# Kernel tuning notes

Hardware: AMD Instinct MI355X
Metric: run time of the kernel (lower is better)

The kernel has to match this reference:

```python
import jax, jax.numpy as jnp
import numpy as np

SHUFFLE_G = 8
NUM_HEADS = 8
EPS = 1e-12


def setup_inputs() -> dict:
    key = jax.random.key(0)
    ks = jax.random.split(key, 7)
    b, dim, t, h, w = 2, 64, 10, 128, 128
    c3 = dim * 3
    return {
        "x": jax.random.normal(ks[0], (b, dim, t, h, w), jnp.float32),
        "W1": jax.random.normal(ks[1], (c3, dim), jnp.float32) * 0.05,            # 1x1x1 conv
        "Wdw": jax.random.normal(ks[2], (c3, 1, 1, 3, 3), jnp.float32) * 0.1,     # depthwise (1,3,3) conv
        "W_lin": jax.random.normal(ks[3], (t * SHUFFLE_G, t * SHUFFLE_G), jnp.float32) * 0.05,
        "b_lin": jax.random.normal(ks[4], (t * SHUFFLE_G,), jnp.float32) * 0.01,
        "temperature": jnp.ones((NUM_HEADS, 1, 1), jnp.float32),
        "W_out": jax.random.normal(ks[5], (dim, dim), jnp.float32) * 0.05,        # 1x1x1 conv
    }


def _l2norm(v):
    n = jnp.sqrt(jnp.sum(v * v, axis=-1, keepdims=True))
    return v / jnp.maximum(n, EPS)


def reference(x, W1, Wdw, W_lin, b_lin, temperature, W_out):
    b, c, t, h, w = x.shape
    c3 = 3 * c
    heads = NUM_HEADS
    # 1x1x1 pointwise conv (no bias)
    y = jnp.einsum('oc,bcthw->bothw', W1, x)
    # depthwise (1,3,3) conv, padding (0,1,1)
    y = jax.lax.conv_general_dilated(
        y, Wdw, window_strides=(1, 1, 1),
        padding=((0, 0), (1, 1), (1, 1)),
        dimension_numbers=('NCDHW', 'OIDHW', 'NCDHW'),
        feature_group_count=c3)
    # shuffle: b (c1 c2) t h w -> b c2 h w (c1 t), c1 = SHUFFLE_G
    c1, c2 = SHUFFLE_G, c3 // SHUFFLE_G
    y = y.reshape(b, c1, c2, t, h, w).transpose(0, 2, 4, 5, 1, 3).reshape(b, c2, h, w, c1 * t)
    # linear mixing along (c1 t)
    y = jnp.einsum('bchwi,oi->bchwo', y, W_lin) + b_lin
    # unshuffle: b c2 h w (c1 t) -> b (c2 c1 t) h w
    y = y.reshape(b, c2, h, w, c1, t).transpose(0, 1, 4, 5, 2, 3).reshape(b, c3 * t, h, w)
    # split qkv along channel
    q, k, v = jnp.split(y, 3, axis=1)  # each [b, c*t, h, w]
    ct, hw = (c // heads) * t, h * w
    q = q.reshape(b, heads, ct, hw)
    k = k.reshape(b, heads, ct, hw)
    v = v.reshape(b, heads, ct, hw)
    q = _l2norm(q)
    k = _l2norm(k)
    attn = jnp.einsum('bhcd,bhed->bhce', q, k) * temperature  # [b, heads, ct, ct]
    attn = jax.nn.softmax(attn, axis=-1)
    out = jnp.einsum('bhce,bhed->bhcd', attn, v)  # [b, heads, ct, hw]
    out = out.reshape(b, c, t, h, w)
    out = jnp.einsum('oc,bcthw->bothw', W_out, out)
    return out
```

## Files before the change

### kernel.cpp

```cpp
#include <hip/hip_runtime.h>
#include <hip/hip_bf16.h>

#define C_  64
#define C3_ 192
#define T_  10
#define H_  128
#define W_  128
#define HW_ 16384
#define THW_ 163840
#define NH_ 8
#define C2_ 24
#define TG_ 80

typedef __hip_bfloat16 bf16;
typedef __attribute__((ext_vector_type(8))) short bf16x8;
typedef __attribute__((ext_vector_type(4))) float f32x4;

__device__ __forceinline__ float bf2f(bf16 v) { return __bfloat162float(v); }

__device__ __forceinline__ ushort f2bf_s(float f) {
  bf16 h = __float2bfloat16(f);
  union { bf16 b; ushort s; } u; u.b = h; return u.s;
}

__device__ __forceinline__ ushort4 pack4(f32x4 a) {
  ushort4 p;
  p.x = f2bf_s(a[0]); p.y = f2bf_s(a[1]); p.z = f2bf_s(a[2]); p.w = f2bf_s(a[3]);
  return p;
}

__device__ __forceinline__ uint pack2lo(uint x, uint y) { return (x & 0xffffu) | (y << 16); }
__device__ __forceinline__ uint pack2hi(uint x, uint y) { return (x >> 16) | (y & 0xffff0000u); }

__device__ __forceinline__ void twrite(char* lds, int stride, int nkc,
                                       uint r[8][4], int kc, int cg) {
#pragma unroll
  for (int j = 0; j < 8; ++j) {
    const int d = j >> 1;
    uint4 o;
    if (j & 1) {
      o.x = pack2hi(r[0][d], r[1][d]); o.y = pack2hi(r[2][d], r[3][d]);
      o.z = pack2hi(r[4][d], r[5][d]); o.w = pack2hi(r[6][d], r[7][d]);
    } else {
      o.x = pack2lo(r[0][d], r[1][d]); o.y = pack2lo(r[2][d], r[3][d]);
      o.z = pack2lo(r[4][d], r[5][d]); o.w = pack2lo(r[6][d], r[7][d]);
    }
    const int col = cg * 8 + j;
    const int rr = (kc + col) % nkc;
    *reinterpret_cast<uint4*>(lds + col * stride + rr * 16) = o;
  }
}

__global__ __launch_bounds__(256) void kprep(
    const float* __restrict__ W1, const float* __restrict__ W_lin,
    const float* __restrict__ W_out,
    bf16* __restrict__ W1bf, bf16* __restrict__ Wlinbf, bf16* __restrict__ Woutbf) {
  const int idx = blockIdx.x * 256 + threadIdx.x;
  if (idx < 12288) {
    W1bf[idx] = __float2bfloat16(W1[idx]);
  } else if (idx < 12288 + 7680) {
    const int i = idx - 12288;
    const int row = i / 96, col = i - row * 96;
    Wlinbf[i] = __float2bfloat16(col < 80 ? W_lin[row * 80 + col] : 0.f);
  } else if (idx < 12288 + 7680 + 4096) {
    const int i = idx - 12288 - 7680;
    Woutbf[i] = __float2bfloat16(W_out[i]);
  }
}

#define K1_TPB 4
__global__ __launch_bounds__(256) void k1_mfma(
    const float* __restrict__ x, const bf16* __restrict__ W1bf,
    bf16* __restrict__ y1ws) {
  __shared__ __align__(16) float xs[2][64 * 128];
  const int tid = threadIdx.x;
  const int lane = tid & 63, wv = tid >> 6;
  const int lr = lane & 15, lg = lane >> 4;
  const int mh = blockIdx.y;
  const int b = blockIdx.z;
  const float* xb = x + (size_t)b * C_ * THW_;
  bf16* y1 = y1ws + (size_t)b * C3_ * THW_;
  const int tile0 = blockIdx.x * K1_TPB;

  const int ro = lane >> 5, colo = (lane & 31) * 4;
  auto STAGE = [&](int buf, int tIdx) {
    const int n0 = tIdx * 128;
#pragma unroll
    for (int i = 0; i < 8; ++i) {
      const int row = wv * 16 + i * 2;
      const float* gsrc = xb + (size_t)(row + ro) * THW_ + n0 + colo;
      __builtin_amdgcn_global_load_lds(
          (const __attribute__((address_space(1))) void*)gsrc,
          (__attribute__((address_space(3))) void*)&xs[buf][row * 128],
          16, 0, 0);
    }
  };

  STAGE(0, tile0);

  bf16x8 wf[6][2];
#pragma unroll
  for (int mt = 0; mt < 6; ++mt)
#pragma unroll
    for (int c = 0; c < 2; ++c) {
      const int row = mh * 96 + mt * 16 + lr;
      wf[mt][c] = *reinterpret_cast<const bf16x8*>(W1bf + row * 64 + c * 32 + lg * 8);
    }
  __syncthreads();

  int buf = 0;
  for (int t = 0; t < K1_TPB; ++t) {
    if (t + 1 < K1_TPB) STAGE(buf ^ 1, tile0 + t + 1);
    const int n0 = (tile0 + t) * 128;
#pragma unroll
    for (int nt = 0; nt < 2; ++nt) {
      const int col = wv * 32 + nt * 16 + lr;
      bf16x8 xa[2];
#pragma unroll
      for (int c = 0; c < 2; ++c) {
        const float* base = &xs[buf][(c * 32 + lg * 8) * 128 + col];
        bf16x8 f;
#pragma unroll
        for (int e = 0; e < 8; ++e) f[e] = f2bf_s(base[e * 128]);
        xa[c] = f;
      }
      f32x4 acc[6];
#pragma unroll
      for (int mt = 0; mt < 6; ++mt) acc[mt] = (f32x4){0.f, 0.f, 0.f, 0.f};
#pragma unroll
      for (int c = 0; c < 2; ++c)
#pragma unroll
        for (int mt = 0; mt < 6; ++mt)
          acc[mt] = __builtin_amdgcn_mfma_f32_16x16x32_bf16(xa[c], wf[mt][c], acc[mt], 0, 0, 0);
      const int nb = n0 + wv * 32 + nt * 16 + lg * 4;
#pragma unroll
      for (int mt = 0; mt < 6; ++mt) {
        const int o = mh * 96 + mt * 16 + lr;
        *reinterpret_cast<ushort4*>(y1 + (size_t)o * THW_ + nb) = pack4(acc[mt]);
      }
    }
    __syncthreads();
    buf ^= 1;
  }
}

__global__ __launch_bounds__(256) void k2_dw(
    const bf16* __restrict__ y1ws, const float* __restrict__ Wdw,
    bf16* __restrict__ y2ws) {
  __shared__ float tile[34][132];
  const int tid = threadIdx.x;
  const int blk = blockIdx.x;
  const int b = blockIdx.y;
  const bf16* y1 = y1ws + (size_t)b * C3_ * THW_;
  bf16* y2 = y2ws + (size_t)b * C3_ * THW_;
  const int hs = (blk & 3) * 32;
  const int rest = blk >> 2;
  const int t = rest % T_;
  const int o = rest / T_;
  const bf16* src = y1 + ((size_t)o * T_ + t) * HW_;

  if (tid < 68) {
    const int r = tid >> 1, side = tid & 1;
    tile[r][side ? 129 : 0] = 0.f;
  }
  {
    const int rr = tid >> 5, c4 = (tid & 31) * 4;
#pragma unroll
    for (int p = 0; p < 5; ++p) {
      const int r = p * 8 + rr;
      if (r < 34) {
        const int hh = hs - 1 + r;
        float e0 = 0.f, e1 = 0.f, e2 = 0.f, e3 = 0.f;
        if (hh >= 0 && hh < H_) {
          uint2 raw = *reinterpret_cast<const uint2*>(src + hh * W_ + c4);
          e0 = __uint_as_float(raw.x << 16);
          e1 = __uint_as_float(raw.x & 0xffff0000u);
          e2 = __uint_as_float(raw.y << 16);
          e3 = __uint_as_float(raw.y & 0xffff0000u);
        }
        tile[r][1 + c4]     = e0;
        tile[r][1 + c4 + 1] = e1;
        tile[r][1 + c4 + 2] = e2;
        tile[r][1 + c4 + 3] = e3;
      }
    }
  }
  __syncthreads();

  float kk[9];
#pragma unroll
  for (int i = 0; i < 9; ++i) kk[i] = Wdw[o * 9 + i];

  bf16* dst = y2 + ((size_t)o * T_ + t) * HW_;
  const int w = tid & 127;
  const int r0 = (tid >> 7) * 16;

  float a[3][3];
#pragma unroll
  for (int ky = 0; ky < 3; ++ky)
#pragma unroll
    for (int kx = 0; kx < 3; ++kx) a[ky][kx] = tile[r0 + ky][w + kx];

#pragma unroll
  for (int q = 0; q < 16; ++q) {
    float acc = 0.f;
#pragma unroll
    for (int ky = 0; ky < 3; ++ky)
#pragma unroll
      for (int kx = 0; kx < 3; ++kx)
        acc = fmaf(kk[ky * 3 + kx], a[ky][kx], acc);
    dst[(hs + r0 + q) * W_ + w] = __float2bfloat16(acc);
    if (q < 15) {
#pragma unroll
      for (int kx = 0; kx < 3; ++kx) {
        a[0][kx] = a[1][kx];
        a[1][kx] = a[2][kx];
        a[2][kx] = tile[r0 + q + 3][w + kx];
      }
    }
  }
}

#define K3_NKC 13
#define K3_STRIDE 208
#define K3_TPB 4
__global__ __launch_bounds__(256) void k3_mfma(
    const bf16* __restrict__ y2ws, const bf16* __restrict__ Wlinbf,
    const float* __restrict__ b_lin, bf16* __restrict__ zws,
    float* __restrict__ ssqws) {
  __shared__ __align__(16) char lds[256 * K3_STRIDE];
  const int tid = threadIdx.x;
  const int tile0 = blockIdx.x * K3_TPB;
  const int c2 = blockIdx.y;
  const int b = blockIdx.z;
  const bf16* y2 = y2ws + (size_t)b * C3_ * THW_;
  bf16* z = zws + (size_t)b * C3_ * THW_;
  float* ssq = ssqws + b * 1280;

  const int lane = tid & 63, wv = tid >> 6;
  const int lr = lane & 15, lg = lane >> 4;

  const int kcA = tid >> 5, cgA = tid & 31;
  const bool hasB = (tid & 3) == 0;
  const int qB = tid >> 2;
  const int kcB = 8 + (qB >> 5), cgB = qB & 31;

  uint rrA[8][4], rrB[8][4];
  auto LOAD = [&](int s0, uint r[8][4], int kc, int cg) {
#pragma unroll
    for (int e = 0; e < 8; ++e) {
      const int k = kc * 8 + e;
      const int c1 = (k * 205) >> 11;
      const int tt = k - c1 * 10;
      uint4 raw = *reinterpret_cast<const uint4*>(
          y2 + ((size_t)((c1 * C2_ + c2) * T_ + tt)) * HW_ + s0 + cg * 8);
      r[e][0] = raw.x; r[e][1] = raw.y; r[e][2] = raw.z; r[e][3] = raw.w;
    }
  };

  LOAD(tile0 * 256, rrA, kcA, cgA);
  if (hasB) LOAD(tile0 * 256, rrB, kcB, cgB);
  {
    const int col = tid;
    const uint4 zero4 = {0, 0, 0, 0};
    *reinterpret_cast<uint4*>(lds + col * K3_STRIDE + ((10 + col) % K3_NKC) * 16) = zero4;
    *reinterpret_cast<uint4*>(lds + col * K3_STRIDE + ((11 + col) % K3_NKC) * 16) = zero4;
  }

  bf16x8 wf[5][3];
#pragma unroll
  for (int mt = 0; mt < 5; ++mt)
#pragma unroll
    for (int c = 0; c < 3; ++c)
      wf[mt][c] = *reinterpret_cast<const bf16x8*>(
          Wlinbf + (mt * 16 + lr) * 96 + c * 32 + lg * 8);
  float bias[5];
#pragma unroll
  for (int mt = 0; mt < 5; ++mt) bias[mt] = b_lin[mt * 16 + lr];

  float sqp[5] = {0.f, 0.f, 0.f, 0.f, 0.f};

#pragma unroll
  for (int t = 0; t < K3_TPB; ++t) {
    const int s0 = (tile0 + t) * 256;
    twrite(lds, K3_STRIDE, K3_NKC, rrA, kcA, cgA);
    if (hasB) twrite(lds, K3_STRIDE, K3_NKC, rrB, kcB, cgB);
    if (t + 1 < K3_TPB) {
      LOAD(s0 + 256, rrA, kcA, cgA);
      if (hasB) LOAD(s0 + 256, rrB, kcB, cgB);
    }
    __syncthreads();

    for (int nt = 0; nt < 4; ++nt) {
      const int col = wv * 64 + nt * 16 + lr;
      bf16x8 xa[3];
#pragma unroll
      for (int c = 0; c < 3; ++c) {
        const int kc = c * 4 + lg;
        xa[c] = *reinterpret_cast<const bf16x8*>(
            lds + col * K3_STRIDE + ((kc + col) % K3_NKC) * 16);
      }
      f32x4 acc[5];
#pragma unroll
      for (int mt = 0; mt < 5; ++mt)
        acc[mt] = (f32x4){bias[mt], bias[mt], bias[mt], bias[mt]};
#pragma unroll
      for (int c = 0; c < 3; ++c)
#pragma unroll
        for (int mt = 0; mt < 5; ++mt)
          acc[mt] = __builtin_amdgcn_mfma_f32_16x16x32_bf16(xa[c], wf[mt][c], acc[mt], 0, 0, 0);
      const int sb = s0 + wv * 64 + nt * 16 + lg * 4;
#pragma unroll
      for (int mt = 0; mt < 5; ++mt) {
        const int u = c2 * TG_ + mt * 16 + lr;
        *reinterpret_cast<ushort4*>(z + (size_t)u * HW_ + sb) = pack4(acc[mt]);
#pragma unroll
        for (int j = 0; j < 4; ++j)
          sqp[mt] = fmaf(acc[mt][j], acc[mt][j], sqp[mt]);
      }
    }
    __syncthreads();
  }

  if (c2 < 16) {
#pragma unroll
    for (int mt = 0; mt < 5; ++mt) {
      float v = sqp[mt];
      v += __shfl_xor(v, 16);
      v += __shfl_xor(v, 32);
      if (lane < 16)
        atomicAdd(&ssq[c2 * TG_ + mt * 16 + lane], v);
    }
  }
}

__global__ __launch_bounds__(256) void k5_mfma(
    const bf16* __restrict__ zws, float* __restrict__ Gpartws) {
  __shared__ __align__(16) float gbuf[2][TG_ * TG_];
  const int chunk = blockIdx.x, h = blockIdx.y, b = blockIdx.z;
  const bf16* z = zws + (size_t)b * C3_ * THW_;
  float* Gpart = Gpartws + (size_t)b * 1638400;
  const int tid = threadIdx.x;
  const int lane = tid & 63, wv = tid >> 6;
  const int lr = lane & 15, lg = lane >> 4;

  const bf16* qbase = z + (size_t)(h * TG_) * HW_;
  const bf16* kbase = z + (size_t)((8 + h) * TG_) * HW_;

  f32x4 acc[5][5];
#pragma unroll
  for (int a = 0; a < 5; ++a)
#pragma unroll
    for (int b2 = 0; b2 < 5; ++b2) acc[a][b2] = (f32x4){0.f, 0.f, 0.f, 0.f};

  const int s0 = chunk * 512 + wv * 128;
  for (int s = s0; s < s0 + 128; s += 32) {
    bf16x8 qa[5], kb[5];
#pragma unroll
    for (int a = 0; a < 5; ++a)
      qa[a] = *reinterpret_cast<const bf16x8*>(qbase + (size_t)(a * 16 + lr) * HW_ + s + lg * 8);
#pragma unroll
    for (int a = 0; a < 5; ++a)
      kb[a] = *reinterpret_cast<const bf16x8*>(kbase + (size_t)(a * 16 + lr) * HW_ + s + lg * 8);
#pragma unroll
    for (int a = 0; a < 5; ++a)
#pragma unroll
      for (int b2 = 0; b2 < 5; ++b2)
        acc[a][b2] = __builtin_amdgcn_mfma_f32_16x16x32_bf16(qa[a], kb[b2], acc[a][b2], 0, 0, 0);
  }

  if (wv == 1 || wv == 3) {
    float* dst = gbuf[wv >> 1];
#pragma unroll
    for (int a = 0; a < 5; ++a)
#pragma unroll
      for (int b2 = 0; b2 < 5; ++b2)
#pragma unroll
        for (int j = 0; j < 4; ++j)
          dst[(a * 16 + lg * 4 + j) * TG_ + b2 * 16 + lr] = acc[a][b2][j];
  }
  __syncthreads();
  if (wv == 0 || wv == 2) {
    const float* srcb = gbuf[wv >> 1];
#pragma unroll
    for (int a = 0; a < 5; ++a)
#pragma unroll
      for (int b2 = 0; b2 < 5; ++b2)
#pragma unroll
        for (int j = 0; j < 4; ++j)
          acc[a][b2][j] += srcb[(a * 16 + lg * 4 + j) * TG_ + b2 * 16 + lr];
  }
  __syncthreads();
  if (wv == 2) {
#pragma unroll
    for (int a = 0; a < 5; ++a)
#pragma unroll
      for (int b2 = 0; b2 < 5; ++b2)
#pragma unroll
        for (int j = 0; j < 4; ++j)
          gbuf[0][(a * 16 + lg * 4 + j) * TG_ + b2 * 16 + lr] = acc[a][b2][j];
  }
  __syncthreads();
  if (wv == 0) {
    float* gp = Gpart + ((size_t)chunk * 8 + h) * TG_ * TG_;
#pragma unroll
    for (int a = 0; a < 5; ++a)
#pragma unroll
      for (int b2 = 0; b2 < 5; ++b2)
#pragma unroll
        for (int j = 0; j < 4; ++j) {
          const int i = a * 16 + lg * 4 + j, jj = b2 * 16 + lr;
          gp[i * TG_ + jj] = acc[a][b2][j] + gbuf[0][i * TG_ + jj];
        }
  }
}

__global__ __launch_bounds__(128) void k6_softmax(
    const float* __restrict__ Gpartws, const float* __restrict__ ssqws,
    const float* __restrict__ temp, bf16* __restrict__ attnbfws) {
  __shared__ float red[128];
  __shared__ float smax, ssum;
  const int b = blockIdx.y;
  const float* Gpart = Gpartws + (size_t)b * 1638400;
  const float* ssq = ssqws + b * 1280;
  bf16* attnbf = attnbfws + (size_t)b * NH_ * TG_ * 96;
  int h = blockIdx.x / TG_, i = blockIdx.x % TG_;
  int j = threadIdx.x;
  float logit = -1e30f;
  if (j < TG_) {
    float g = 0.f;
    for (int c = 0; c < 32; ++c)
      g += Gpart[(((size_t)c * 8 + h) * TG_ + i) * TG_ + j];
    float nq = ssq[h * TG_ + i];
    float nk = ssq[(8 + h) * TG_ + j];
    float sq = 1.f / fmaxf(sqrtf(nq), 1e-12f);
    float sk = 1.f / fmaxf(sqrtf(nk), 1e-12f);
    logit = g * sq * sk * temp[h];
  }
  red[j] = logit;
  __syncthreads();
  if (j == 0) {
    float m = -1e30f;
    for (int x2 = 0; x2 < TG_; ++x2) m = fmaxf(m, red[x2]);
    smax = m;
  }
  __syncthreads();
  float e = (j < TG_) ? expf(logit - smax) : 0.f;
  red[j] = e;
  __syncthreads();
  if (j == 0) {
    float s = 0.f;
    for (int x2 = 0; x2 < TG_; ++x2) s += red[x2];
    ssum = s;
  }
  __syncthreads();
  if (j < 96)
    attnbf[((size_t)h * TG_ + i) * 96 + j] =
        __float2bfloat16(j < TG_ ? e / ssum : 0.f);
}

#define K7A_TPB 4
__global__ __launch_bounds__(256) void k7a_mfma(
    const bf16* __restrict__ zws, const bf16* __restrict__ attnbfws,
    bf16* __restrict__ att_outws) {
  __shared__ __align__(16) char lds[256 * K3_STRIDE];
  const int tid = threadIdx.x;
  const int tile0 = blockIdx.x * K7A_TPB;
  const int h = blockIdx.y;
  const int b = blockIdx.z;
  const bf16* z = zws + (size_t)b * C3_ * THW_;
  const bf16* attnbf = attnbfws + (size_t)b * NH_ * TG_ * 96;
  bf16* att_out = att_outws + (size_t)b * NH_ * TG_ * HW_;
  const int voff = (16 + h) * TG_;

  const int lane = tid & 63, wv = tid >> 6;
  const int lr = lane & 15, lg = lane >> 4;

  const int kcA = tid >> 5, cgA = tid & 31;
  const bool hasB = (tid & 3) == 0;
  const int qB = tid >> 2;
  const int kcB = 8 + (qB >> 5), cgB = qB & 31;

  uint rrA[8][4], rrB[8][4];
  auto LOAD = [&](int s0, uint r[8][4], int kc, int cg) {
#pragma unroll
    for (int e = 0; e < 8; ++e) {
      uint4 raw = *reinterpret_cast<const uint4*>(
          z + (size_t)(voff + kc * 8 + e) * HW_ + s0 + cg * 8);
      r[e][0] = raw.x; r[e][1] = raw.y; r[e][2] = raw.z; r[e][3] = raw.w;
    }
  };

  LOAD(tile0 * 256, rrA, kcA, cgA);
  if (hasB) LOAD(tile0 * 256, rrB, kcB, cgB);
  {
    const int col = tid;
    const uint4 zero4 = {0, 0, 0, 0};
    *reinterpret_cast<uint4*>(lds + col * K3_STRIDE + ((10 + col) % K3_NKC) * 16) = zero4;
    *reinterpret_cast<uint4*>(lds + col * K3_STRIDE + ((11 + col) % K3_NKC) * 16) = zero4;
  }

  bf16x8 wf[5][3];
#pragma unroll
  for (int mt = 0; mt < 5; ++mt)
#pragma unroll
    for (int c = 0; c < 3; ++c)
      wf[mt][c] = *reinterpret_cast<const bf16x8*>(
          attnbf + ((size_t)h * TG_ + mt * 16 + lr) * 96 + c * 32 + lg * 8);

#pragma unroll
  for (int t = 0; t < K7A_TPB; ++t) {
    const int s0 = (tile0 + t) * 256;
    twrite(lds, K3_STRIDE, K3_NKC, rrA, kcA, cgA);
    if (hasB) twrite(lds, K3_STRIDE, K3_NKC, rrB, kcB, cgB);
    if (t + 1 < K7A_TPB) {
      LOAD(s0 + 256, rrA, kcA, cgA);
      if (hasB) LOAD(s0 + 256, rrB, kcB, cgB);
    }
    __syncthreads();

    for (int nt = 0; nt < 4; ++nt) {
      const int col = wv * 64 + nt * 16 + lr;
      bf16x8 xa[3];
#pragma unroll
      for (int c = 0; c < 3; ++c) {
        const int kc = c * 4 + lg;
        xa[c] = *reinterpret_cast<const bf16x8*>(
            lds + col * K3_STRIDE + ((kc + col) % K3_NKC) * 16);
      }
      f32x4 acc[5];
#pragma unroll
      for (int mt = 0; mt < 5; ++mt) acc[mt] = (f32x4){0.f, 0.f, 0.f, 0.f};
#pragma unroll
      for (int c = 0; c < 3; ++c)
#pragma unroll
        for (int mt = 0; mt < 5; ++mt)
          acc[mt] = __builtin_amdgcn_mfma_f32_16x16x32_bf16(xa[c], wf[mt][c], acc[mt], 0, 0, 0);
      const int sb = s0 + wv * 64 + nt * 16 + lg * 4;
#pragma unroll
      for (int mt = 0; mt < 5; ++mt) {
        const int u = h * TG_ + mt * 16 + lr;
        *reinterpret_cast<ushort4*>(att_out + (size_t)u * HW_ + sb) = pack4(acc[mt]);
      }
    }
    __syncthreads();
  }
}

#define K1_NKC 10
#define K1_STRIDE 160
#define K7B_TPB 4
__global__ __launch_bounds__(256) void k7b_mfma(
    const bf16* __restrict__ att_outws, const bf16* __restrict__ Woutbf,
    float* __restrict__ out) {
  __shared__ __align__(16) char lds[256 * K1_STRIDE];
  const int tid = threadIdx.x;
  const int tile0 = blockIdx.x * K7B_TPB;
  const int b = blockIdx.y;
  const bf16* att_out = att_outws + (size_t)b * NH_ * TG_ * HW_;
  float* outb = out + (size_t)b * C_ * THW_;
  const int t_ = tile0 >> 6;
  const int lane = tid & 63, wv = tid >> 6;
  const int lr = lane & 15, lg = lane >> 4;

  const int kcA = tid >> 5, cgA = tid & 31;
  uint rrA[8][4];
  auto LOAD = [&](int tile, uint r[8][4]) {
    const int sb0 = (tile * 256) & (HW_ - 1);
#pragma unroll
    for (int e = 0; e < 8; ++e) {
      const int row = kcA * TG_ + e * T_ + t_;
      uint4 raw = *reinterpret_cast<const uint4*>(
          att_out + (size_t)row * HW_ + sb0 + cgA * 8);
      r[e][0] = raw.x; r[e][1] = raw.y; r[e][2] = raw.z; r[e][3] = raw.w;
    }
  };

  LOAD(tile0, rrA);

  bf16x8 wf[4][2];
#pragma unroll
  for (int mt = 0; mt < 4; ++mt)
#pragma unroll
    for (int c = 0; c < 2; ++c)
      wf[mt][c] = *reinterpret_cast<const bf16x8*>(
          Woutbf + (mt * 16 + lr) * 64 + c * 32 + lg * 8);

#pragma unroll
  for (int t = 0; t < K7B_TPB; ++t) {
    const int n0 = (tile0 + t) * 256;
    twrite(lds, K1_STRIDE, K1_NKC, rrA, kcA, cgA);
    if (t + 1 < K7B_TPB) LOAD(tile0 + t + 1, rrA);
    __syncthreads();

    for (int nt = 0; nt < 4; ++nt) {
      const int col = wv * 64 + nt * 16 + lr;
      bf16x8 xa[2];
#pragma unroll
      for (int c = 0; c < 2; ++c) {
        const int kc = c * 4 + lg;
        xa[c] = *reinterpret_cast<const bf16x8*>(
            lds + col * K1_STRIDE + ((kc + col) % K1_NKC) * 16);
      }
      f32x4 acc[4];
#pragma unroll
      for (int mt = 0; mt < 4; ++mt) acc[mt] = (f32x4){0.f, 0.f, 0.f, 0.f};
#pragma unroll
      for (int c = 0; c < 2; ++c)
#pragma unroll
        for (int mt = 0; mt < 4; ++mt)
          acc[mt] = __builtin_amdgcn_mfma_f32_16x16x32_bf16(xa[c], wf[mt][c], acc[mt], 0, 0, 0);
      const int nb = n0 + wv * 64 + nt * 16 + lg * 4;
#pragma unroll
      for (int mt = 0; mt < 4; ++mt) {
        const int o = mt * 16 + lr;
        *reinterpret_cast<float4*>(outb + (size_t)o * THW_ + nb) =
            (float4){acc[mt][0], acc[mt][1], acc[mt][2], acc[mt][3]};
      }
    }
    __syncthreads();
  }
}

extern "C" void kernel_launch(void* const* d_in, const int* in_sizes, int n_in,
                              void* d_out, int out_size, void* d_ws, size_t ws_size,
                              hipStream_t stream) {
  const float* x    = (const float*)d_in[0];
  const float* W1   = (const float*)d_in[1];
  const float* Wdw  = (const float*)d_in[2];
  const float* Wlin = (const float*)d_in[3];
  const float* blin = (const float*)d_in[4];
  const float* temp = (const float*)d_in[5];
  const float* Wout = (const float*)d_in[6];
  float* out = (float*)d_out;

  const size_t NY = (size_t)C3_ * THW_;
  char* ws = (char*)d_ws;
  bf16* y1z = (bf16*)ws;
  bf16* y2  = (bf16*)(ws + 4 * NY);
  char* E   = ws + 8 * NY;
  float* Gpart  = (float*)E;
  bf16* attnbf  = (bf16*)(E + 13107200);
  bf16* att_out = (bf16*)(E + 13352960);
  float* ssq    = (float*)(E + 55296000);
  bf16* W1bf    = (bf16*)(E + 55306240);
  bf16* Wlinbf  = (bf16*)(E + 55330816);
  bf16* Woutbf  = (bf16*)(E + 55346176);

  kprep<<<94, 256, 0, stream>>>(W1, Wlin, Wout, W1bf, Wlinbf, Woutbf);
  hipMemsetAsync(ssq, 0, 2 * 1280 * sizeof(float), stream);
  k1_mfma<<<dim3(THW_ / 128 / K1_TPB, 2, 2), 256, 0, stream>>>(x, W1bf, y1z);
  k2_dw<<<dim3(C3_ * T_ * 4, 2), 256, 0, stream>>>(y1z, Wdw, y2);
  k3_mfma<<<dim3(HW_ / 256 / K3_TPB, C2_, 2), 256, 0, stream>>>(y2, Wlinbf, blin, y1z, ssq);
  k5_mfma<<<dim3(32, NH_, 2), 256, 0, stream>>>(y1z, Gpart);
  k6_softmax<<<dim3(NH_ * TG_, 2), 128, 0, stream>>>(Gpart, ssq, temp, attnbf);
  k7a_mfma<<<dim3(HW_ / 256 / K7A_TPB, NH_, 2), 256, 0, stream>>>(y1z, attnbf, att_out);
  k7b_mfma<<<dim3(THW_ / 256 / K7B_TPB, 2), 256, 0, stream>>>(att_out, Woutbf, out);
}
```

Before: 284.9 us.

## Stage k1 input as bf16 via registers into swizzled LDS; move syncs before prefetch

```diff
diff --git a/kernel.cpp b/kernel.cpp
--- a/kernel.cpp
+++ b/kernel.cpp
@@ -68,35 +68,40 @@
   }
 }
 
+#define K1_NKC 10
+#define K1_STRIDE 160
 #define K1_TPB 4
 __global__ __launch_bounds__(256) void k1_mfma(
     const float* __restrict__ x, const bf16* __restrict__ W1bf,
     bf16* __restrict__ y1ws) {
-  __shared__ __align__(16) float xs[2][64 * 128];
+  __shared__ __align__(16) char lds[256 * K1_STRIDE];
   const int tid = threadIdx.x;
-  const int lane = tid & 63, wv = tid >> 6;
-  const int lr = lane & 15, lg = lane >> 4;
+  const int tile0 = blockIdx.x * K1_TPB;
   const int mh = blockIdx.y;
   const int b = blockIdx.z;
   const float* xb = x + (size_t)b * C_ * THW_;
   bf16* y1 = y1ws + (size_t)b * C3_ * THW_;
-  const int tile0 = blockIdx.x * K1_TPB;
-
-  const int ro = lane >> 5, colo = (lane & 31) * 4;
-  auto STAGE = [&](int buf, int tIdx) {
-    const int n0 = tIdx * 128;
-#pragma unroll
-    for (int i = 0; i < 8; ++i) {
-      const int row = wv * 16 + i * 2;
-      const float* gsrc = xb + (size_t)(row + ro) * THW_ + n0 + colo;
-      __builtin_amdgcn_global_load_lds(
-          (const __attribute__((address_space(1))) void*)gsrc,
-          (__attribute__((address_space(3))) void*)&xs[buf][row * 128],
-          16, 0, 0);
+
+  const int lane = tid & 63, wv = tid >> 6;
+  const int lr = lane & 15, lg = lane >> 4;
+  const int kcA = tid >> 5, cgA = tid & 31;
+
+  uint rrA[8][4];
+  auto LOAD = [&](int s0) {
+#pragma unroll
+    for (int e = 0; e < 8; ++e) {
+      const int k = kcA * 8 + e;
+      const float* src = xb + (size_t)k * THW_ + s0 + cgA * 8;
+      float4 f0 = *reinterpret_cast<const float4*>(src);
+      float4 f1 = *reinterpret_cast<const float4*>(src + 4);
+      rrA[e][0] = (uint)f2bf_s(f0.x) | ((uint)f2bf_s(f0.y) << 16);
+      rrA[e][1] = (uint)f2bf_s(f0.z) | ((uint)f2bf_s(f0.w) << 16);
+      rrA[e][2] = (uint)f2bf_s(f1.x) | ((uint)f2bf_s(f1.y) << 16);
+      rrA[e][3] = (uint)f2bf_s(f1.z) | ((uint)f2bf_s(f1.w) << 16);
     }
   };
 
-  STAGE(0, tile0);
+  LOAD(tile0 * 256);
 
   bf16x8 wf[6][2];
 #pragma unroll
@@ -106,23 +111,22 @@
       const int row = mh * 96 + mt * 16 + lr;
       wf[mt][c] = *reinterpret_cast<const bf16x8*>(W1bf + row * 64 + c * 32 + lg * 8);
     }
-  __syncthreads();
-
-  int buf = 0;
+
+#pragma unroll
   for (int t = 0; t < K1_TPB; ++t) {
-    if (t + 1 < K1_TPB) STAGE(buf ^ 1, tile0 + t + 1);
-    const int n0 = (tile0 + t) * 128;
-#pragma unroll
-    for (int nt = 0; nt < 2; ++nt) {
-      const int col = wv * 32 + nt * 16 + lr;
+    const int s0 = (tile0 + t) * 256;
+    twrite(lds, K1_STRIDE, K1_NKC, rrA, kcA, cgA);
+    __syncthreads();
+    if (t + 1 < K1_TPB) LOAD(s0 + 256);
+
+    for (int nt = 0; nt < 4; ++nt) {
+      const int col = wv * 64 + nt * 16 + lr;
       bf16x8 xa[2];
 #pragma unroll
       for (int c = 0; c < 2; ++c) {
-        const float* base = &xs[buf][(c * 32 + lg * 8) * 128 + col];
-        bf16x8 f;
-#pragma unroll
-        for (int e = 0; e < 8; ++e) f[e] = f2bf_s(base[e * 128]);
-        xa[c] = f;
+        const int kc = c * 4 + lg;
+        xa[c] = *reinterpret_cast<const bf16x8*>(
+            lds + col * K1_STRIDE + ((kc + col) % K1_NKC) * 16);
       }
       f32x4 acc[6];
 #pragma unroll
@@ -132,7 +136,7 @@
 #pragma unroll
         for (int mt = 0; mt < 6; ++mt)
           acc[mt] = __builtin_amdgcn_mfma_f32_16x16x32_bf16(xa[c], wf[mt][c], acc[mt], 0, 0, 0);
-      const int nb = n0 + wv * 32 + nt * 16 + lg * 4;
+      const int nb = s0 + wv * 64 + nt * 16 + lg * 4;
 #pragma unroll
       for (int mt = 0; mt < 6; ++mt) {
         const int o = mh * 96 + mt * 16 + lr;
@@ -140,7 +144,6 @@
       }
     }
     __syncthreads();
-    buf ^= 1;
   }
 }
 
@@ -285,11 +288,11 @@
     const int s0 = (tile0 + t) * 256;
     twrite(lds, K3_STRIDE, K3_NKC, rrA, kcA, cgA);
     if (hasB) twrite(lds, K3_STRIDE, K3_NKC, rrB, kcB, cgB);
+    __syncthreads();
     if (t + 1 < K3_TPB) {
       LOAD(s0 + 256, rrA, kcA, cgA);
       if (hasB) LOAD(s0 + 256, rrB, kcB, cgB);
     }
-    __syncthreads();
 
     for (int nt = 0; nt < 4; ++nt) {
       const int col = wv * 64 + nt * 16 + lr;
@@ -513,11 +516,11 @@
     const int s0 = (tile0 + t) * 256;
     twrite(lds, K3_STRIDE, K3_NKC, rrA, kcA, cgA);
     if (hasB) twrite(lds, K3_STRIDE, K3_NKC, rrB, kcB, cgB);
+    __syncthreads();
     if (t + 1 < K7A_TPB) {
       LOAD(s0 + 256, rrA, kcA, cgA);
       if (hasB) LOAD(s0 + 256, rrB, kcB, cgB);
     }
-    __syncthreads();
 
     for (int nt = 0; nt < 4; ++nt) {
       const int col = wv * 64 + nt * 16 + lr;
@@ -547,8 +550,6 @@
   }
 }
 
-#define K1_NKC 10
-#define K1_STRIDE 160
 #define K7B_TPB 4
 __global__ __launch_bounds__(256) void k7b_mfma(
     const bf16* __restrict__ att_outws, const bf16* __restrict__ Woutbf,
@@ -590,8 +591,8 @@
   for (int t = 0; t < K7B_TPB; ++t) {
     const int n0 = (tile0 + t) * 256;
     twrite(lds, K1_STRIDE, K1_NKC, rrA, kcA, cgA);
+    __syncthreads();
     if (t + 1 < K7B_TPB) LOAD(tile0 + t + 1, rrA);
-    __syncthreads();
 
     for (int nt = 0; nt < 4; ++nt) {
       const int col = wv * 64 + nt * 16 + lr;
@@ -649,7 +650,7 @@
 
   kprep<<<94, 256, 0, stream>>>(W1, Wlin, Wout, W1bf, Wlinbf, Woutbf);
   hipMemsetAsync(ssq, 0, 2 * 1280 * sizeof(float), stream);
-  k1_mfma<<<dim3(THW_ / 128 / K1_TPB, 2, 2), 256, 0, stream>>>(x, W1bf, y1z);
+  k1_mfma<<<dim3(THW_ / 256 / K1_TPB, 2, 2), 256, 0, stream>>>(x, W1bf, y1z);
   k2_dw<<<dim3(C3_ * T_ * 4, 2), 256, 0, stream>>>(y1z, Wdw, y2);
   k3_mfma<<<dim3(HW_ / 256 / K3_TPB, C2_, 2), 256, 0, stream>>>(y2, Wlinbf, blin, y1z, ssq);
   k5_mfma<<<dim3(32, NH_, 2), 256, 0, stream>>>(y1z, Gpart);
```

New measurement: 306.0 us. +7.4%, slower.
